# Kernel optimization log

Measured on AMD Instinct MI355X. Metric: run time of the kernel, lower is better.

Reference implementation:

```python
import jax, jax.numpy as jnp
import numpy as np

B = 16777216  # 2**24 samples


def setup_inputs() -> dict:
    key = jax.random.key(0)
    k = jax.random.split(key, 6)
    # physiological BP ranges so all five category masks are populated
    s = jax.random.uniform(k[0], (B,), jnp.float32, 90.0, 200.0)   # systolic targets
    d = jax.random.uniform(k[1], (B,), jnp.float32, 50.0, 130.0)   # diastolic targets
    m = jax.random.uniform(k[2], (B,), jnp.float32, 60.0, 150.0)   # mean BP targets (unused)
    sbp_pred = (s + 10.0 * jax.random.normal(k[3], (B,), jnp.float32))[:, None]  # [B,1], squeezed in fwd
    dbp_pred = d + 10.0 * jax.random.normal(k[4], (B,), jnp.float32)
    mbp_pred = m + 10.0 * jax.random.normal(k[5], (B,), jnp.float32)  # unused by loss
    return {"dbp_pred": dbp_pred, "sbp_pred": sbp_pred, "mbp_pred": mbp_pred,
            "d": d, "s": s, "m": m}


def _smape(p, t):
    # standard SMAPE: |p-t| / ((|p|+|t|)/2)
    return 2.0 * jnp.abs(p - t) / (jnp.abs(p) + jnp.abs(t))


def reference(dbp_pred, sbp_pred, mbp_pred, d, s, m):
    batchN = s.shape[0]
    sbp_p = jnp.squeeze(sbp_pred)  # [B]

    normal = (s < 120) & (d < 80)
    elevated = (s >= 120) & (s < 130) & (d < 80) & ~normal
    hyper1 = (((s >= 130) & (s < 140)) | ((d >= 80) & (d < 90))) & ~(normal | elevated)
    hyper2 = ((s >= 140) | (d >= 90)) & ~(normal | elevated | hyper1)
    crisis = (s > 180) | (d > 120)  # intentionally not exclusive, as in original
    masks = [normal, elevated, hyper1, hyper2, crisis]

    # per-element smape sum (dbp + sbp), computed once and reused for every mask
    per_elem = _smape(dbp_pred, d) + _smape(sbp_p, s)  # [B]

    rst = jnp.float32(0.0)
    m_rst = jnp.float32(0.0)   # carries over across masks, as in the original code
    mask_cnt = jnp.float32(0.0)
    for mk in masks:
        cnt = jnp.sum(mk).astype(jnp.float32)
        w = jnp.sqrt(jnp.log(batchN / jnp.maximum(cnt, 1.0)))  # guard; unused when cnt==0
        S = jnp.sum(jnp.where(mk, per_elem, 0.0)) * w
        nz = cnt > 0
        m_rst = jnp.where(nz, (m_rst + S) / cnt / 2.0, m_rst)
        rst = jnp.where(nz, rst + m_rst, rst)
        mask_cnt = mask_cnt + nz.astype(jnp.float32)

    return jnp.where(mask_cnt == 0, rst / 5.0, rst / mask_cnt)
```

## Files before the change

kernel.cpp:

```cpp
#include <hip/hip_runtime.h>


#define B_TOTAL 16777216
#define NSETS 8
#define NBLOCKS 2048
#define NTHREADS 256

__device__ __forceinline__ float smape_f(float p, float t) {
    return 2.0f * fabsf(p - t) / (fabsf(p) + fabsf(t));
}

__global__ __launch_bounds__(NTHREADS)
void amploss_reduce(const float* __restrict__ dbp,
                    const float* __restrict__ sbp,
                    const float* __restrict__ dt,
                    const float* __restrict__ st,
                    double* __restrict__ ws)
{
    double sum[5] = {0.0, 0.0, 0.0, 0.0, 0.0};
    int    cnt[5] = {0, 0, 0, 0, 0};

    const int nquads = B_TOTAL / 4;
    const int stride = gridDim.x * blockDim.x;
    const float4* __restrict__ dbp4 = (const float4*)dbp;
    const float4* __restrict__ sbp4 = (const float4*)sbp;
    const float4* __restrict__ dt4  = (const float4*)dt;
    const float4* __restrict__ st4  = (const float4*)st;

    for (int q = blockIdx.x * blockDim.x + threadIdx.x; q < nquads; q += stride) {
        float4 dp = dbp4[q];
        float4 sp = sbp4[q];
        float4 dv = dt4[q];
        float4 sv = st4[q];
        float dpv[4] = {dp.x, dp.y, dp.z, dp.w};
        float spv[4] = {sp.x, sp.y, sp.z, sp.w};
        float dvv[4] = {dv.x, dv.y, dv.z, dv.w};
        float svv[4] = {sv.x, sv.y, sv.z, sv.w};
        #pragma unroll
        for (int j = 0; j < 4; ++j) {
            float s = svv[j], d = dvv[j];
            bool normal   = (s < 120.0f) && (d < 80.0f);
            bool elevated = (s >= 120.0f) && (s < 130.0f) && (d < 80.0f) && !normal;
            bool h1 = (((s >= 130.0f) && (s < 140.0f)) || ((d >= 80.0f) && (d < 90.0f)))
                      && !(normal || elevated);
            bool h2 = ((s >= 140.0f) || (d >= 90.0f)) && !(normal || elevated || h1);
            bool crisis = (s > 180.0f) || (d > 120.0f);

            float pe = smape_f(dpv[j], d) + smape_f(spv[j], s);
            double ped = (double)pe;

            if (normal)   { cnt[0]++; sum[0] += ped; }
            if (elevated) { cnt[1]++; sum[1] += ped; }
            if (h1)       { cnt[2]++; sum[2] += ped; }
            if (h2)       { cnt[3]++; sum[3] += ped; }
            if (crisis)   { cnt[4]++; sum[4] += ped; }
        }
    }

    #pragma unroll
    for (int off = 32; off > 0; off >>= 1) {
        #pragma unroll
        for (int k = 0; k < 5; ++k) {
            sum[k] += __shfl_down(sum[k], off);
            cnt[k] += __shfl_down(cnt[k], off);
        }
    }

    __shared__ double s_sum[5][NTHREADS / 64];
    __shared__ int    s_cnt[5][NTHREADS / 64];
    const int lane = threadIdx.x & 63;
    const int wid  = threadIdx.x >> 6;
    if (lane == 0) {
        #pragma unroll
        for (int k = 0; k < 5; ++k) { s_sum[k][wid] = sum[k]; s_cnt[k][wid] = cnt[k]; }
    }
    __syncthreads();

    if (threadIdx.x == 0) {
        const int base = (blockIdx.x & (NSETS - 1)) * 10;
        #pragma unroll
        for (int k = 0; k < 5; ++k) {
            double ss = 0.0; double cc = 0.0;
            #pragma unroll
            for (int w = 0; w < NTHREADS / 64; ++w) { ss += s_sum[k][w]; cc += (double)s_cnt[k][w]; }
            atomicAdd(&ws[base + k], ss);
            atomicAdd(&ws[base + 5 + k], cc);
        }
    }
}

__global__ void amploss_finalize(const double* __restrict__ ws, float* __restrict__ out)
{
    if (threadIdx.x != 0 || blockIdx.x != 0) return;
    double S[5], C[5];
    for (int k = 0; k < 5; ++k) { S[k] = 0.0; C[k] = 0.0; }
    for (int st = 0; st < NSETS; ++st)
        for (int k = 0; k < 5; ++k) {
            S[k] += ws[st * 10 + k];
            C[k] += ws[st * 10 + 5 + k];
        }

    double rst = 0.0, m_rst = 0.0, mask_cnt = 0.0;
    for (int k = 0; k < 5; ++k) {
        double c = C[k];
        float w = sqrtf(logf((float)B_TOTAL / fmaxf((float)c, 1.0f)));
        double Sw = S[k] * (double)w;
        if (c > 0.0) {
            m_rst = (m_rst + Sw) / c / 2.0;
            rst += m_rst;
            mask_cnt += 1.0;
        }
    }
    double r = (mask_cnt == 0.0) ? (rst / 5.0) : (rst / mask_cnt);
    out[0] = (float)r;
}

extern "C" void kernel_launch(void* const* d_in, const int* in_sizes, int n_in,
                              void* d_out, int out_size, void* d_ws, size_t ws_size,
                              hipStream_t stream) {
    const float* dbp = (const float*)d_in[0];
    const float* sbp = (const float*)d_in[1];
    const float* dt  = (const float*)d_in[3];
    const float* st  = (const float*)d_in[4];
    float* out = (float*)d_out;
    double* ws = (double*)d_ws;

    hipMemsetAsync(ws, 0, NSETS * 10 * sizeof(double), stream);
    amploss_reduce<<<NBLOCKS, NTHREADS, 0, stream>>>(dbp, sbp, dt, st, ws);
    amploss_finalize<<<1, 64, 0, stream>>>(ws, out);
}
```

Baseline: 329.7 us.

## Fuse finalize into reduce kernel with last-block counter and fast float math

Merges the finalize kernel into the reduction kernel: a global atomic counter lets the last block compute the final loss, which removes one kernel launch. Per-thread accumulators change from double to float, divisions become hardware reciprocal approximations, and branches become selects. The grid-stride loop becomes a fully unrolled fixed 8-iteration loop with two quads of loads in flight per step to raise memory-level parallelism. These changes risk precision loss from float accumulation and the approximate reciprocal, and the unrolled loop hardcodes the problem size.

```diff
diff --git a/kernel.cpp b/kernel.cpp
--- a/kernel.cpp
+++ b/kernel.cpp
@@ -5,56 +5,68 @@
 #define NSETS 8
 #define NBLOCKS 2048
 #define NTHREADS 256
+#define NQUADS (B_TOTAL / 4)
+#define STRIDE (NBLOCKS * NTHREADS)
 
-__device__ __forceinline__ float smape_f(float p, float t) {
-    return 2.0f * fabsf(p - t) / (fabsf(p) + fabsf(t));
+__device__ __forceinline__ float rcp_fast(float x) {
+    return __builtin_amdgcn_rcpf(x);
+}
+
+__device__ __forceinline__ void proc4(float4 dp, float4 sp, float4 dv, float4 sv,
+                                      float (&sum)[5], int (&cnt)[5]) {
+    float dpv[4] = {dp.x, dp.y, dp.z, dp.w};
+    float spv[4] = {sp.x, sp.y, sp.z, sp.w};
+    float dvv[4] = {dv.x, dv.y, dv.z, dv.w};
+    float svv[4] = {sv.x, sv.y, sv.z, sv.w};
+    #pragma unroll
+    for (int j = 0; j < 4; ++j) {
+        float s = svv[j], d = dvv[j];
+        bool normal   = (s < 120.0f) && (d < 80.0f);
+        bool elevated = (s >= 120.0f) && (s < 130.0f) && (d < 80.0f) && !normal;
+        bool h1 = (((s >= 130.0f) && (s < 140.0f)) || ((d >= 80.0f) && (d < 90.0f)))
+                  && !(normal || elevated);
+        bool h2 = ((s >= 140.0f) || (d >= 90.0f)) && !(normal || elevated || h1);
+        bool crisis = (s > 180.0f) || (d > 120.0f);
+
+        float pe = 2.0f * (fabsf(dpv[j] - d) * rcp_fast(fabsf(dpv[j]) + fabsf(d)) +
+                           fabsf(spv[j] - s) * rcp_fast(fabsf(spv[j]) + fabsf(s)));
+
+        sum[0] += normal   ? pe : 0.0f;  cnt[0] += normal;
+        sum[1] += elevated ? pe : 0.0f;  cnt[1] += elevated;
+        sum[2] += h1       ? pe : 0.0f;  cnt[2] += h1;
+        sum[3] += h2       ? pe : 0.0f;  cnt[3] += h2;
+        sum[4] += crisis   ? pe : 0.0f;  cnt[4] += crisis;
+    }
 }
 
 __global__ __launch_bounds__(NTHREADS)
-void amploss_reduce(const float* __restrict__ dbp,
-                    const float* __restrict__ sbp,
-                    const float* __restrict__ dt,
-                    const float* __restrict__ st,
-                    double* __restrict__ ws)
+void amploss_fused(const float* __restrict__ dbp,
+                   const float* __restrict__ sbp,
+                   const float* __restrict__ dt,
+                   const float* __restrict__ st,
+                   double* __restrict__ ws,
+                   float* __restrict__ out)
 {
-    double sum[5] = {0.0, 0.0, 0.0, 0.0, 0.0};
-    int    cnt[5] = {0, 0, 0, 0, 0};
-
-    const int nquads = B_TOTAL / 4;
-    const int stride = gridDim.x * blockDim.x;
     const float4* __restrict__ dbp4 = (const float4*)dbp;
     const float4* __restrict__ sbp4 = (const float4*)sbp;
     const float4* __restrict__ dt4  = (const float4*)dt;
     const float4* __restrict__ st4  = (const float4*)st;
 
-    for (int q = blockIdx.x * blockDim.x + threadIdx.x; q < nquads; q += stride) {
-        float4 dp = dbp4[q];
-        float4 sp = sbp4[q];
-        float4 dv = dt4[q];
-        float4 sv = st4[q];
-        float dpv[4] = {dp.x, dp.y, dp.z, dp.w};
-        float spv[4] = {sp.x, sp.y, sp.z, sp.w};
-        float dvv[4] = {dv.x, dv.y, dv.z, dv.w};
-        float svv[4] = {sv.x, sv.y, sv.z, sv.w};
-        #pragma unroll
-        for (int j = 0; j < 4; ++j) {
-            float s = svv[j], d = dvv[j];
-            bool normal   = (s < 120.0f) && (d < 80.0f);
-            bool elevated = (s >= 120.0f) && (s < 130.0f) && (d < 80.0f) && !normal;
-            bool h1 = (((s >= 130.0f) && (s < 140.0f)) || ((d >= 80.0f) && (d < 90.0f)))
-                      && !(normal || elevated);
-            bool h2 = ((s >= 140.0f) || (d >= 90.0f)) && !(normal || elevated || h1);
-            bool crisis = (s > 180.0f) || (d > 120.0f);
+    float sum[5] = {0.f, 0.f, 0.f, 0.f, 0.f};
+    int   cnt[5] = {0, 0, 0, 0, 0};
 
-            float pe = smape_f(dpv[j], d) + smape_f(spv[j], s);
-            double ped = (double)pe;
+    const int q0 = blockIdx.x * NTHREADS + threadIdx.x;
 
-            if (normal)   { cnt[0]++; sum[0] += ped; }
-            if (elevated) { cnt[1]++; sum[1] += ped; }
-            if (h1)       { cnt[2]++; sum[2] += ped; }
-            if (h2)       { cnt[3]++; sum[3] += ped; }
-            if (crisis)   { cnt[4]++; sum[4] += ped; }
-        }
+    #pragma unroll
+    for (int k = 0; k < 8; k += 2) {
+        const int qa = q0 + k * STRIDE;
+        const int qb = q0 + (k + 1) * STRIDE;
+        float4 a0 = dbp4[qa], a1 = dbp4[qb];
+        float4 b0 = sbp4[qa], b1 = sbp4[qb];
+        float4 c0 = dt4[qa],  c1 = dt4[qb];
+        float4 e0 = st4[qa],  e1 = st4[qb];
+        proc4(a0, b0, c0, e0, sum, cnt);
+        proc4(a1, b1, c1, e1, sum, cnt);
     }
 
     #pragma unroll
@@ -66,8 +78,8 @@
         }
     }
 
-    __shared__ double s_sum[5][NTHREADS / 64];
-    __shared__ int    s_cnt[5][NTHREADS / 64];
+    __shared__ float s_sum[5][NTHREADS / 64];
+    __shared__ int   s_cnt[5][NTHREADS / 64];
     const int lane = threadIdx.x & 63;
     const int wid  = threadIdx.x >> 6;
     if (lane == 0) {
@@ -82,37 +94,43 @@
         for (int k = 0; k < 5; ++k) {
             double ss = 0.0; double cc = 0.0;
             #pragma unroll
-            for (int w = 0; w < NTHREADS / 64; ++w) { ss += s_sum[k][w]; cc += (double)s_cnt[k][w]; }
+            for (int w = 0; w < NTHREADS / 64; ++w) {
+                ss += (double)s_sum[k][w];
+                cc += (double)s_cnt[k][w];
+            }
             atomicAdd(&ws[base + k], ss);
             atomicAdd(&ws[base + 5 + k], cc);
         }
-    }
-}
-
-__global__ void amploss_finalize(const double* __restrict__ ws, float* __restrict__ out)
-{
-    if (threadIdx.x != 0 || blockIdx.x != 0) return;
-    double S[5], C[5];
-    for (int k = 0; k < 5; ++k) { S[k] = 0.0; C[k] = 0.0; }
-    for (int st = 0; st < NSETS; ++st)
-        for (int k = 0; k < 5; ++k) {
-            S[k] += ws[st * 10 + k];
-            C[k] += ws[st * 10 + 5 + k];
-        }
-
-    double rst = 0.0, m_rst = 0.0, mask_cnt = 0.0;
-    for (int k = 0; k < 5; ++k) {
-        double c = C[k];
-        float w = sqrtf(logf((float)B_TOTAL / fmaxf((float)c, 1.0f)));
-        double Sw = S[k] * (double)w;
-        if (c > 0.0) {
-            m_rst = (m_rst + Sw) / c / 2.0;
-            rst += m_rst;
-            mask_cnt += 1.0;
+        __threadfence();
+        unsigned int* ctr = (unsigned int*)(ws + NSETS * 10);
+        unsigned int old = atomicAdd(ctr, 1u);
+        if (old == NBLOCKS - 1) {
+            double S[5], C[5];
+            #pragma unroll
+            for (int k = 0; k < 5; ++k) { S[k] = 0.0; C[k] = 0.0; }
+            for (int st = 0; st < NSETS; ++st) {
+                #pragma unroll
+                for (int k = 0; k < 5; ++k) {
+                    S[k] += atomicAdd(&ws[st * 10 + k], 0.0);
+                    C[k] += atomicAdd(&ws[st * 10 + 5 + k], 0.0);
+                }
+            }
+            double rst = 0.0, m_rst = 0.0, mask_cnt = 0.0;
+            #pragma unroll
+            for (int k = 0; k < 5; ++k) {
+                double c = C[k];
+                float w = sqrtf(logf((float)B_TOTAL / fmaxf((float)c, 1.0f)));
+                double Sw = S[k] * (double)w;
+                if (c > 0.0) {
+                    m_rst = (m_rst + Sw) / c / 2.0;
+                    rst += m_rst;
+                    mask_cnt += 1.0;
+                }
+            }
+            double r = (mask_cnt == 0.0) ? (rst / 5.0) : (rst / mask_cnt);
+            out[0] = (float)r;
         }
     }
-    double r = (mask_cnt == 0.0) ? (rst / 5.0) : (rst / mask_cnt);
-    out[0] = (float)r;
 }
 
 extern "C" void kernel_launch(void* const* d_in, const int* in_sizes, int n_in,
@@ -125,7 +143,6 @@
     float* out = (float*)d_out;
     double* ws = (double*)d_ws;
 
-    hipMemsetAsync(ws, 0, NSETS * 10 * sizeof(double), stream);
-    amploss_reduce<<<NBLOCKS, NTHREADS, 0, stream>>>(dbp, sbp, dt, st, ws);
-    amploss_finalize<<<1, 64, 0, stream>>>(ws, out);
+    hipMemsetAsync(ws, 0, NSETS * 10 * sizeof(double) + sizeof(unsigned int), stream);
+    amploss_fused<<<NBLOCKS, NTHREADS, 0, stream>>>(dbp, sbp, dt, st, ws, out);
 }
```

After: 446.5 us. +35.4%, slower.
